# Kernel tuning notes

Measured on AMD Instinct MI355X. Metric: run time of the kernel, lower is better.

## Reference

```python
import jax, jax.numpy as jnp
import numpy as np

# --- model constants (cfg stand-ins) ---
V_TH = 1.0        # spike threshold
SURR_BETA = 0.2   # surrogate-gradient sigmoid slope
ALPHA_MEM = 0.9   # membrane leak
STP_DECAY = 0.95  # short-term plasticity recovery
STP_R = 0.3       # STP depression per spike
A_P = 0.01        # STDP potentiation amplitude (Abbott)
A_D = 0.012       # STDP depression amplitude (Abbott)

B, N, N_FF, D = 16, 2048, 512, 4  # batch, recurrent neurons, FF inputs, delays


def setup_inputs() -> dict:
    key = jax.random.key(0)
    ks = jax.random.split(key, 10)
    FF = jax.random.uniform(ks[0], (B, N_FF), dtype=jnp.float32)          # feedforward spikes/rates
    V = jax.random.normal(ks[1], (B, N), dtype=jnp.float32) * 0.5         # membrane potential
    th_adapt = jax.random.uniform(ks[2], (B, N), dtype=jnp.float32) * 0.2 # adaptive threshold (ALIF)
    Xbuf = (jax.random.uniform(ks[3], (D, B, N)) < 0.05).astype(jnp.float32)  # delayed spike buffer
    stp_state = jax.random.uniform(ks[4], (D, B, N), dtype=jnp.float32) * 0.1 - 0.05
    xbar_pre_int = jax.random.uniform(ks[5], (B, N), dtype=jnp.float32)   # presyn STDP trace (int)
    xbar_post = jax.random.uniform(ks[6], (B, N), dtype=jnp.float32)      # postsyn STDP trace
    xbar_pre_ff = jax.random.uniform(ks[7], (B, N_FF), dtype=jnp.float32) # presyn STDP trace (ff)
    W_int = jax.random.normal(ks[8], (N, N), dtype=jnp.float32) / np.sqrt(N)
    W_ff = jax.random.normal(ks[9], (N_FF, N), dtype=jnp.float32) / np.sqrt(N_FF)
    return dict(FF=FF, V=V, th_adapt=th_adapt, Xbuf=Xbuf, stp_state=stp_state,
                xbar_pre_int=xbar_pre_int, xbar_post=xbar_post, xbar_pre_ff=xbar_pre_ff,
                W_int=W_int, W_ff=W_ff)


def reference(FF, V, th_adapt, Xbuf, stp_state, xbar_pre_int, xbar_post, xbar_pre_ff, W_int, W_ff):
    # ALIFSpikes: spikes from membrane vs adaptive threshold (sigmoid surrogate),
    # delayed spikes Xd read from the circular buffer.
    X = jax.nn.sigmoid((V - (V_TH + th_adapt)) / SURR_BETA)          # [B,N]
    Xd = Xbuf                                                        # [D,B,N]

    # STP: per-presynaptic, per-delay short-term weight factor
    w_short = 1.0 + (stp_state * STP_DECAY - STP_R * Xd)             # [D,B,N]

    # Abbott STDP: pairwise pre/post trace modulation of base weights
    # w_long[b,i,j] = W[i,j] + A_P*xbar_pre[b,i]*X[b,j] - A_D*pre_spike[b,i]*xbar_post[b,j]
    w_long_int = (W_int[None]
                  + A_P * xbar_pre_int[:, :, None] * X[:, None, :]
                  - A_D * Xd[0][:, :, None] * xbar_post[:, None, :])  # [B,N,N]
    w_long_ff = (W_ff[None]
                 + A_P * xbar_pre_ff[:, :, None] * X[:, None, :]
                 - A_D * FF[:, :, None] * xbar_post[:, None, :])      # [B,N_FF,N]

    # DeltaSynapse: spike-gated, STP-modulated current accumulation
    current = (jnp.einsum('dbi,bij->bj', Xd * w_short, w_long_int)
               + jnp.einsum('bi,bij->bj', FF, w_long_ff))             # [B,N]

    # Membrane: leaky integration with reset-by-spike
    V_new = ALPHA_MEM * V * (1.0 - X) + current                      # [B,N]

    return jnp.stack([X, V_new])                                     # [2,B,N]
```

## Files before the change

### kernel.cpp

```cpp
#include <hip/hip_runtime.h>

#define BB 16
#define NN 2048
#define NFF 512
#define DD 4

#define ROWS 64
#define WR 16
#define YINT 32
#define YTOT 40
#define JC   256

__global__ __launch_bounds__(256) void snn_pre(
    const float* __restrict__ FF, const float* __restrict__ V,
    const float* __restrict__ th, const float* __restrict__ Xbuf,
    const float* __restrict__ stp, const float* __restrict__ xpre_int,
    const float* __restrict__ xpre_ff,
    float* __restrict__ out_X, float* __restrict__ T,
    float* __restrict__ scal_part)
{
    __shared__ float red[8];
    int idx = blockIdx.x * 256 + threadIdx.x;
    float p0, p1;
    if (idx < BB * NN) {
        float v = V[idx], t = th[idx];
        float x = 1.f / (1.f + expf(-(v - 1.f - t) * 5.f));
        out_X[idx] = x;
        float xd0 = Xbuf[idx];
        float acc = 0.f;
        #pragma unroll
        for (int d = 0; d < DD; ++d) {
            float xd = Xbuf[d * BB * NN + idx];
            float s  = stp[d * BB * NN + idx];
            acc += xd * (1.f + 0.95f * s - 0.3f * xd);
        }
        T[idx] = acc;
        p0 = acc * xpre_int[idx];
        p1 = acc * xd0;
    } else {
        int k = idx - BB * NN;
        float f = FF[k];
        p0 = f * xpre_ff[k];
        p1 = f * f;
    }
    #pragma unroll
    for (int o = 32; o; o >>= 1) { p0 += __shfl_xor(p0, o); p1 += __shfl_xor(p1, o); }
    int w = threadIdx.x >> 6;
    if ((threadIdx.x & 63) == 0) { red[w * 2] = p0; red[w * 2 + 1] = p1; }
    __syncthreads();
    if (threadIdx.x == 0) {
        scal_part[blockIdx.x * 2]     = red[0] + red[2] + red[4] + red[6];
        scal_part[blockIdx.x * 2 + 1] = red[1] + red[3] + red[5] + red[7];
    }
}

__global__ __launch_bounds__(256) void snn_gemv(
    const float* __restrict__ Wint, const float* __restrict__ Wff,
    const float* __restrict__ T, const float* __restrict__ FF,
    float* __restrict__ part)
{
    __shared__ float  c_lds[ROWS * BB];
    __shared__ float4 red[2 * BB * 64];
    int y = blockIdx.y;
    const float* Wm; const float* OP; int i0, opstride;
    if (y < YINT) { Wm = Wint; OP = T;  i0 = y * ROWS;          opstride = NN;  }
    else          { Wm = Wff;  OP = FF; i0 = (y - YINT) * ROWS; opstride = NFF; }

    int t = threadIdx.x;
    #pragma unroll
    for (int k = 0; k < ROWS * BB / 256; ++k) {
        int e = k * 256 + t;
        int row = e >> 4, b = e & 15;
        c_lds[e] = OP[b * opstride + i0 + row];
    }
    __syncthreads();

    int w = t >> 6, l = t & 63;
    int j0 = blockIdx.x * JC + l * 4;

    const float* wp = Wm + (size_t)(i0 + w * WR) * NN + j0;
    float4 buf[WR];
    #pragma unroll
    for (int r = 0; r < WR; ++r) buf[r] = *(const float4*)(wp + (size_t)r * NN);

    float4 acc[BB];
    #pragma unroll
    for (int b = 0; b < BB; ++b) acc[b] = make_float4(0.f, 0.f, 0.f, 0.f);

    #pragma unroll
    for (int r = 0; r < WR; ++r) {
        const float4* cb = (const float4*)&c_lds[(w * WR + r) * BB];
        float4 c0 = cb[0], c1 = cb[1], c2 = cb[2], c3 = cb[3];
        float4 wv = buf[r];
#define FMA4(b, cc) acc[b].x += (cc) * wv.x; acc[b].y += (cc) * wv.y; \
                    acc[b].z += (cc) * wv.z; acc[b].w += (cc) * wv.w;
        FMA4(0,  c0.x) FMA4(1,  c0.y) FMA4(2,  c0.z) FMA4(3,  c0.w)
        FMA4(4,  c1.x) FMA4(5,  c1.y) FMA4(6,  c1.z) FMA4(7,  c1.w)
        FMA4(8,  c2.x) FMA4(9,  c2.y) FMA4(10, c2.z) FMA4(11, c2.w)
        FMA4(12, c3.x) FMA4(13, c3.y) FMA4(14, c3.z) FMA4(15, c3.w)
#undef FMA4
    }

    if (w >= 2) {
        float4* rb = &red[(w - 2) * BB * 64];
        #pragma unroll
        for (int b = 0; b < BB; ++b) rb[b * 64 + l] = acc[b];
    }
    __syncthreads();
    if (w < 2) {
        const float4* rb = &red[w * BB * 64];
        #pragma unroll
        for (int b = 0; b < BB; ++b) {
            float4 v = rb[b * 64 + l];
            acc[b].x += v.x; acc[b].y += v.y; acc[b].z += v.z; acc[b].w += v.w;
        }
    }
    __syncthreads();
    if (w == 1) {
        #pragma unroll
        for (int b = 0; b < BB; ++b) red[b * 64 + l] = acc[b];
    }
    __syncthreads();
    if (w == 0) {
        float* pp = part + (size_t)y * (BB * NN) + j0;
        #pragma unroll
        for (int b = 0; b < BB; ++b) {
            float4 v = red[b * 64 + l];
            acc[b].x += v.x; acc[b].y += v.y; acc[b].z += v.z; acc[b].w += v.w;
            *(float4*)(pp + (size_t)b * NN) = acc[b];
        }
    }
}

__global__ __launch_bounds__(256) void snn_post(
    const float* __restrict__ V, const float* __restrict__ xpost,
    const float* __restrict__ part, const float* __restrict__ scal_part,
    const float* __restrict__ out_X, float* __restrict__ out_V)
{
    int idx = blockIdx.x * 256 + threadIdx.x;
    int b = idx >> 11;
    float c1 = 0.f, c2 = 0.f, c3 = 0.f, c4 = 0.f;
    #pragma unroll
    for (int k = 0; k < 8; ++k) {
        c1 += scal_part[(b * 8 + k) * 2];
        c2 += scal_part[(b * 8 + k) * 2 + 1];
    }
    #pragma unroll
    for (int k = 0; k < 2; ++k) {
        c3 += scal_part[(128 + b * 2 + k) * 2];
        c4 += scal_part[(128 + b * 2 + k) * 2 + 1];
    }
    float s = 0.f;
    #pragma unroll
    for (int yy = 0; yy < YTOT; ++yy) s += part[(size_t)yy * (BB * NN) + idx];
    float x = out_X[idx];
    float c = s + 0.01f * (c1 + c3) * x - 0.012f * (c2 + c4) * xpost[idx];
    out_V[idx] = 0.9f * V[idx] * (1.f - x) + c;
}

extern "C" void kernel_launch(void* const* d_in, const int* in_sizes, int n_in,
                              void* d_out, int out_size, void* d_ws, size_t ws_size,
                              hipStream_t stream) {
    const float* FF       = (const float*)d_in[0];
    const float* V        = (const float*)d_in[1];
    const float* th       = (const float*)d_in[2];
    const float* Xbuf     = (const float*)d_in[3];
    const float* stp      = (const float*)d_in[4];
    const float* xpre_int = (const float*)d_in[5];
    const float* xpost    = (const float*)d_in[6];
    const float* xpre_ff  = (const float*)d_in[7];
    const float* Wint     = (const float*)d_in[8];
    const float* Wff      = (const float*)d_in[9];
    float* out = (float*)d_out;
    float* ws  = (float*)d_ws;

    float* T    = ws;
    float* part = ws + BB * NN;
    float* sp   = ws + BB * NN + YTOT * BB * NN;

    snn_pre<<<(BB * NN + BB * NFF) / 256, 256, 0, stream>>>(
        FF, V, th, Xbuf, stp, xpre_int, xpre_ff, out, T, sp);

    snn_gemv<<<dim3(NN / JC, YTOT), 256, 0, stream>>>(
        Wint, Wff, T, FF, part);

    snn_post<<<BB * NN / 256, 256, 0, stream>>>(
        V, xpost, part, sp, out, out + BB * NN);
}
```

Before: 18.80 us.

## Fuse post-processing into GEMV via atomic accumulation and last-block tail

```diff
diff --git a/kernel.cpp b/kernel.cpp
--- a/kernel.cpp
+++ b/kernel.cpp
@@ -10,6 +10,7 @@
 #define YINT 32
 #define YTOT 40
 #define JC   256
+#define NX   (NN / JC)
 
 __global__ __launch_bounds__(256) void snn_pre(
     const float* __restrict__ FF, const float* __restrict__ V,
@@ -17,15 +18,18 @@
     const float* __restrict__ stp, const float* __restrict__ xpre_int,
     const float* __restrict__ xpre_ff,
     float* __restrict__ out_X, float* __restrict__ T,
-    float* __restrict__ scal_part)
+    float* __restrict__ cur, float* __restrict__ scal_part,
+    unsigned int* __restrict__ cnt)
 {
     __shared__ float red[8];
     int idx = blockIdx.x * 256 + threadIdx.x;
+    if (blockIdx.x == 0 && threadIdx.x < NX) cnt[threadIdx.x] = 0u;
     float p0, p1;
     if (idx < BB * NN) {
         float v = V[idx], t = th[idx];
         float x = 1.f / (1.f + expf(-(v - 1.f - t) * 5.f));
         out_X[idx] = x;
+        cur[idx] = 0.f;
         float xd0 = Xbuf[idx];
         float acc = 0.f;
         #pragma unroll
@@ -57,10 +61,15 @@
 __global__ __launch_bounds__(256) void snn_gemv(
     const float* __restrict__ Wint, const float* __restrict__ Wff,
     const float* __restrict__ T, const float* __restrict__ FF,
-    float* __restrict__ part)
+    const float* __restrict__ V, const float* __restrict__ xpost,
+    const float* __restrict__ scal_part, const float* __restrict__ out_X,
+    float* __restrict__ out_V, float* __restrict__ cur,
+    unsigned int* __restrict__ cnt)
 {
     __shared__ float  c_lds[ROWS * BB];
     __shared__ float4 red[2 * BB * 64];
+    __shared__ unsigned int tail_flag;
+    __shared__ float csum[4 * BB];
     int y = blockIdx.y;
     const float* Wm; const float* OP; int i0, opstride;
     if (y < YINT) { Wm = Wint; OP = T;  i0 = y * ROWS;          opstride = NN;  }
@@ -122,40 +131,49 @@
     }
     __syncthreads();
     if (w == 0) {
-        float* pp = part + (size_t)y * (BB * NN) + j0;
+        float* pp = cur + j0;
         #pragma unroll
         for (int b = 0; b < BB; ++b) {
             float4 v = red[b * 64 + l];
-            acc[b].x += v.x; acc[b].y += v.y; acc[b].z += v.z; acc[b].w += v.w;
-            *(float4*)(pp + (size_t)b * NN) = acc[b];
-        }
-    }
-}
-
-__global__ __launch_bounds__(256) void snn_post(
-    const float* __restrict__ V, const float* __restrict__ xpost,
-    const float* __restrict__ part, const float* __restrict__ scal_part,
-    const float* __restrict__ out_X, float* __restrict__ out_V)
-{
-    int idx = blockIdx.x * 256 + threadIdx.x;
-    int b = idx >> 11;
-    float c1 = 0.f, c2 = 0.f, c3 = 0.f, c4 = 0.f;
-    #pragma unroll
-    for (int k = 0; k < 8; ++k) {
-        c1 += scal_part[(b * 8 + k) * 2];
-        c2 += scal_part[(b * 8 + k) * 2 + 1];
-    }
-    #pragma unroll
-    for (int k = 0; k < 2; ++k) {
-        c3 += scal_part[(128 + b * 2 + k) * 2];
-        c4 += scal_part[(128 + b * 2 + k) * 2 + 1];
-    }
-    float s = 0.f;
-    #pragma unroll
-    for (int yy = 0; yy < YTOT; ++yy) s += part[(size_t)yy * (BB * NN) + idx];
-    float x = out_X[idx];
-    float c = s + 0.01f * (c1 + c3) * x - 0.012f * (c2 + c4) * xpost[idx];
-    out_V[idx] = 0.9f * V[idx] * (1.f - x) + c;
+            atomicAdd(pp + (size_t)b * NN + 0, acc[b].x + v.x);
+            atomicAdd(pp + (size_t)b * NN + 1, acc[b].y + v.y);
+            atomicAdd(pp + (size_t)b * NN + 2, acc[b].z + v.z);
+            atomicAdd(pp + (size_t)b * NN + 3, acc[b].w + v.w);
+        }
+    }
+
+    __syncthreads();
+    if (t == 0) {
+        unsigned int old = atomicAdd(&cnt[blockIdx.x], 1u);
+        tail_flag = (old == YTOT - 1) ? 1u : 0u;
+    }
+    __syncthreads();
+    if (!tail_flag) return;
+
+    if (t < 64) {
+        int c = t >> 4, b = t & 15;
+        float s = 0.f;
+        if (c < 2) {
+            #pragma unroll
+            for (int k = 0; k < 8; ++k) s += scal_part[(b * 8 + k) * 2 + c];
+        } else {
+            #pragma unroll
+            for (int k = 0; k < 2; ++k) s += scal_part[(128 + b * 2 + k) * 2 + (c - 2)];
+        }
+        csum[c * BB + b] = s;
+    }
+    __syncthreads();
+
+    int j = blockIdx.x * JC + t;
+    #pragma unroll
+    for (int b = 0; b < BB; ++b) {
+        int idx = b * NN + j;
+        float s = atomicAdd(&cur[idx], 0.0f);
+        float x = out_X[idx];
+        float c = s + 0.01f  * (csum[0 * BB + b] + csum[2 * BB + b]) * x
+                    - 0.012f * (csum[1 * BB + b] + csum[3 * BB + b]) * xpost[idx];
+        out_V[idx] = 0.9f * V[idx] * (1.f - x) + c;
+    }
 }
 
 extern "C" void kernel_launch(void* const* d_in, const int* in_sizes, int n_in,
@@ -175,15 +193,13 @@
     float* ws  = (float*)d_ws;
 
     float* T    = ws;
-    float* part = ws + BB * NN;
-    float* sp   = ws + BB * NN + YTOT * BB * NN;
+    float* cur  = ws + BB * NN;
+    float* sp   = ws + 2 * BB * NN;
+    unsigned int* cnt = (unsigned int*)(sp + 320);
 
     snn_pre<<<(BB * NN + BB * NFF) / 256, 256, 0, stream>>>(
-        FF, V, th, Xbuf, stp, xpre_int, xpre_ff, out, T, sp);
-
-    snn_gemv<<<dim3(NN / JC, YTOT), 256, 0, stream>>>(
-        Wint, Wff, T, FF, part);
-
-    snn_post<<<BB * NN / 256, 256, 0, stream>>>(
-        V, xpost, part, sp, out, out + BB * NN);
+        FF, V, th, Xbuf, stp, xpre_int, xpre_ff, out, T, cur, sp, cnt);
+
+    snn_gemv<<<dim3(NX, YTOT), 256, 0, stream>>>(
+        Wint, Wff, T, FF, V, xpost, sp, out, out + BB * NN, cur, cnt);
 }
```

Result: slower. 42.58 us (+126.5%).

## Fuse pre-pass into GEMV and post kernels, dropping one launch

Applied to the files above, without the earlier changes.

```diff
diff --git a/kernel.cpp b/kernel.cpp
--- a/kernel.cpp
+++ b/kernel.cpp
@@ -4,79 +4,85 @@
 #define NN 2048
 #define NFF 512
 #define DD 4
+#define BN (BB * NN)
 
 #define ROWS 64
 #define WR 16
 #define YINT 32
 #define YTOT 40
 #define JC   256
-
-__global__ __launch_bounds__(256) void snn_pre(
-    const float* __restrict__ FF, const float* __restrict__ V,
-    const float* __restrict__ th, const float* __restrict__ Xbuf,
-    const float* __restrict__ stp, const float* __restrict__ xpre_int,
-    const float* __restrict__ xpre_ff,
-    float* __restrict__ out_X, float* __restrict__ T,
-    float* __restrict__ scal_part)
-{
-    __shared__ float red[8];
-    int idx = blockIdx.x * 256 + threadIdx.x;
-    float p0, p1;
-    if (idx < BB * NN) {
-        float v = V[idx], t = th[idx];
-        float x = 1.f / (1.f + expf(-(v - 1.f - t) * 5.f));
-        out_X[idx] = x;
-        float xd0 = Xbuf[idx];
-        float acc = 0.f;
-        #pragma unroll
-        for (int d = 0; d < DD; ++d) {
-            float xd = Xbuf[d * BB * NN + idx];
-            float s  = stp[d * BB * NN + idx];
-            acc += xd * (1.f + 0.95f * s - 0.3f * xd);
-        }
-        T[idx] = acc;
-        p0 = acc * xpre_int[idx];
-        p1 = acc * xd0;
-    } else {
-        int k = idx - BB * NN;
-        float f = FF[k];
-        p0 = f * xpre_ff[k];
-        p1 = f * f;
-    }
-    #pragma unroll
-    for (int o = 32; o; o >>= 1) { p0 += __shfl_xor(p0, o); p1 += __shfl_xor(p1, o); }
-    int w = threadIdx.x >> 6;
-    if ((threadIdx.x & 63) == 0) { red[w * 2] = p0; red[w * 2 + 1] = p1; }
-    __syncthreads();
-    if (threadIdx.x == 0) {
-        scal_part[blockIdx.x * 2]     = red[0] + red[2] + red[4] + red[6];
-        scal_part[blockIdx.x * 2 + 1] = red[1] + red[3] + red[5] + red[7];
-    }
-}
+#define NX   (NN / JC)
 
 __global__ __launch_bounds__(256) void snn_gemv(
     const float* __restrict__ Wint, const float* __restrict__ Wff,
-    const float* __restrict__ T, const float* __restrict__ FF,
-    float* __restrict__ part)
+    const float* __restrict__ Xbuf, const float* __restrict__ stp,
+    const float* __restrict__ FF,
+    const float* __restrict__ xpre_int, const float* __restrict__ xpre_ff,
+    float* __restrict__ part, float* __restrict__ scal_part)
 {
     __shared__ float  c_lds[ROWS * BB];
     __shared__ float4 red[2 * BB * 64];
-    int y = blockIdx.y;
-    const float* Wm; const float* OP; int i0, opstride;
-    if (y < YINT) { Wm = Wint; OP = T;  i0 = y * ROWS;          opstride = NN;  }
-    else          { Wm = Wff;  OP = FF; i0 = (y - YINT) * ROWS; opstride = NFF; }
+    int x = blockIdx.x, y = blockIdx.y;
+    int t = threadIdx.x;
+    const float* Wm; int i0;
 
-    int t = threadIdx.x;
-    #pragma unroll
-    for (int k = 0; k < ROWS * BB / 256; ++k) {
-        int e = k * 256 + t;
-        int row = e >> 4, b = e & 15;
-        c_lds[e] = OP[b * opstride + i0 + row];
+    if (y < YINT) {
+        i0 = y * ROWS; Wm = Wint;
+        #pragma unroll
+        for (int k = 0; k < ROWS * BB / 256; ++k) {
+            int e = k * 256 + t;
+            int row = e >> 4, b = e & 15;
+            int base = b * NN + i0 + row;
+            float acc = 0.f;
+            #pragma unroll
+            for (int d = 0; d < DD; ++d) {
+                float xd = Xbuf[d * BN + base];
+                float s  = stp[d * BN + base];
+                acc += xd * (1.f + 0.95f * s - 0.3f * xd);
+            }
+            c_lds[e] = acc;
+        }
+    } else {
+        i0 = (y - YINT) * ROWS; Wm = Wff;
+        #pragma unroll
+        for (int k = 0; k < ROWS * BB / 256; ++k) {
+            int e = k * 256 + t;
+            int row = e >> 4, b = e & 15;
+            c_lds[e] = FF[b * NFF + i0 + row];
+        }
     }
     __syncthreads();
 
+    if (x == 0) {
+        int b = t >> 4, rg = t & 15;
+        float s0 = 0.f, s1 = 0.f;
+        if (y < YINT) {
+            #pragma unroll
+            for (int k = 0; k < 4; ++k) {
+                int row = rg * 4 + k;
+                float tv = c_lds[row * BB + b];
+                s0 += tv * xpre_int[b * NN + i0 + row];
+                s1 += tv * Xbuf[b * NN + i0 + row];
+            }
+        } else {
+            #pragma unroll
+            for (int k = 0; k < 4; ++k) {
+                int row = rg * 4 + k;
+                float f = c_lds[row * BB + b];
+                s0 += f * xpre_ff[b * NFF + i0 + row];
+                s1 += f * f;
+            }
+        }
+        #pragma unroll
+        for (int o = 1; o < 16; o <<= 1) { s0 += __shfl_xor(s0, o); s1 += __shfl_xor(s1, o); }
+        if (rg == 0) {
+            scal_part[y * 32 + b]      = s0;
+            scal_part[y * 32 + 16 + b] = s1;
+        }
+    }
+
     int w = t >> 6, l = t & 63;
-    int j0 = blockIdx.x * JC + l * 4;
+    int j0 = x * JC + l * 4;
 
     const float* wp = Wm + (size_t)(i0 + w * WR) * NN + j0;
     float4 buf[WR];
@@ -122,7 +128,7 @@
     }
     __syncthreads();
     if (w == 0) {
-        float* pp = part + (size_t)y * (BB * NN) + j0;
+        float* pp = part + (size_t)y * BN + j0;
         #pragma unroll
         for (int b = 0; b < BB; ++b) {
             float4 v = red[b * 64 + l];
@@ -133,29 +139,32 @@
 }
 
 __global__ __launch_bounds__(256) void snn_post(
-    const float* __restrict__ V, const float* __restrict__ xpost,
+    const float* __restrict__ V, const float* __restrict__ th,
+    const float* __restrict__ xpost,
     const float* __restrict__ part, const float* __restrict__ scal_part,
-    const float* __restrict__ out_X, float* __restrict__ out_V)
+    float* __restrict__ out_X, float* __restrict__ out_V)
 {
     int idx = blockIdx.x * 256 + threadIdx.x;
     int b = idx >> 11;
     float c1 = 0.f, c2 = 0.f, c3 = 0.f, c4 = 0.f;
     #pragma unroll
-    for (int k = 0; k < 8; ++k) {
-        c1 += scal_part[(b * 8 + k) * 2];
-        c2 += scal_part[(b * 8 + k) * 2 + 1];
+    for (int y = 0; y < YINT; ++y) {
+        c1 += scal_part[y * 32 + b];
+        c2 += scal_part[y * 32 + 16 + b];
     }
     #pragma unroll
-    for (int k = 0; k < 2; ++k) {
-        c3 += scal_part[(128 + b * 2 + k) * 2];
-        c4 += scal_part[(128 + b * 2 + k) * 2 + 1];
+    for (int y = YINT; y < YTOT; ++y) {
+        c3 += scal_part[y * 32 + b];
+        c4 += scal_part[y * 32 + 16 + b];
     }
+    float v = V[idx];
+    float x = 1.f / (1.f + expf(-(v - 1.f - th[idx]) * 5.f));
+    out_X[idx] = x;
     float s = 0.f;
     #pragma unroll
-    for (int yy = 0; yy < YTOT; ++yy) s += part[(size_t)yy * (BB * NN) + idx];
-    float x = out_X[idx];
+    for (int y = 0; y < YTOT; ++y) s += part[(size_t)y * BN + idx];
     float c = s + 0.01f * (c1 + c3) * x - 0.012f * (c2 + c4) * xpost[idx];
-    out_V[idx] = 0.9f * V[idx] * (1.f - x) + c;
+    out_V[idx] = 0.9f * v * (1.f - x) + c;
 }
 
 extern "C" void kernel_launch(void* const* d_in, const int* in_sizes, int n_in,
@@ -174,16 +183,12 @@
     float* out = (float*)d_out;
     float* ws  = (float*)d_ws;
 
-    float* T    = ws;
-    float* part = ws + BB * NN;
-    float* sp   = ws + BB * NN + YTOT * BB * NN;
+    float* part = ws;
+    float* sp   = ws + YTOT * BN;
 
-    snn_pre<<<(BB * NN + BB * NFF) / 256, 256, 0, stream>>>(
-        FF, V, th, Xbuf, stp, xpre_int, xpre_ff, out, T, sp);
+    snn_gemv<<<dim3(NX, YTOT), 256, 0, stream>>>(
+        Wint, Wff, Xbuf, stp, FF, xpre_int, xpre_ff, part, sp);
 
-    snn_gemv<<<dim3(NN / JC, YTOT), 256, 0, stream>>>(
-        Wint, Wff, T, FF, part);
-
-    snn_post<<<BB * NN / 256, 256, 0, stream>>>(
-        V, xpost, part, sp, out, out + BB * NN);
+    snn_post<<<BN / 256, 256, 0, stream>>>(
+        V, th, xpost, part, sp, out, out + BN);
 }
```

Measured after the change: 19.42 us. +3.3%, slower.
